# Kernel optimization log

Measured on AMD Instinct MI355X. Metric: run time of the kernel, lower is better.

Reference implementation:

```python
import jax, jax.numpy as jnp
import numpy as np

N = 100000      # nodes
E = 800000      # edges (before self-loops)
G = 128         # graphs
IN = 64         # per-table embedding dim (6 tables -> 384 input features)
L = 128         # layer_embd
OUT = 128       # out_embd
H = 2           # attention heads (concat=False -> mean over heads)
VOCABS = [33, 5, 3, 4, 2, 3]
NEG_SLOPE = 0.2
BN_EPS = 1e-5


def _seg_softmax(logits, seg, n):
    # softmax of per-edge/per-node logits grouped by segment id
    m = jax.ops.segment_max(logits, seg, num_segments=n)
    e = jnp.exp(logits - m[seg])
    s = jax.ops.segment_sum(e, seg, num_segments=n)
    return e / (s[seg] + 1e-16)


def _gat_conv(x, W, a_src, a_dst, b, src, dst, n):
    # PyG GATConv, add_self_loops already applied to (src,dst), concat=False
    h = (x @ W).reshape(n, H, -1)                 # [N,H,C]
    al_s = jnp.sum(h * a_src, axis=-1)            # [N,H]
    al_d = jnp.sum(h * a_dst, axis=-1)            # [N,H]
    e = jax.nn.leaky_relu(al_s[src] + al_d[dst], NEG_SLOPE)   # [E,H]
    alpha = _seg_softmax(e, dst, n)               # softmax over each dst's in-edges
    msg = h[src] * alpha[:, :, None]              # [E,H,C]
    out = jax.ops.segment_sum(msg, dst, num_segments=n)       # [N,H,C]
    return out.mean(axis=1) + b                   # head-mean + bias


def setup_inputs() -> dict:
    key = jax.random.key(0)
    ks = jax.random.split(key, 40)
    cols = [jax.random.randint(ks[i], (N, 1), 0, VOCABS[i]) for i in range(6)]
    x = jnp.concatenate(cols, axis=1).astype(jnp.int64)
    edge_index = jax.random.randint(ks[6], (2, E), 0, N).astype(jnp.int64)
    edge_type = jax.random.randint(ks[7], (E,), 0, 4).astype(jnp.int64)
    batch = jnp.sort(jax.random.randint(ks[8], (N,), 0, G)).astype(jnp.int64)
    s = 0.05
    p = {}
    for i in range(6):
        p[f"emb{i}"] = jax.random.normal(ks[10 + i], (VOCABS[i], IN)) * s
    p["W1"] = jax.random.normal(ks[16], (6 * IN, H * L)) * s
    p["as1"] = jax.random.normal(ks[17], (H, L)) * s
    p["ad1"] = jax.random.normal(ks[18], (H, L)) * s
    p["b1"] = jnp.zeros((L,))
    p["W2"] = jax.random.normal(ks[19], (L, H * OUT)) * s
    p["as2"] = jax.random.normal(ks[20], (H, OUT)) * s
    p["ad2"] = jax.random.normal(ks[21], (H, OUT)) * s
    p["b2"] = jnp.zeros((OUT,))
    p["gw1"] = jax.random.normal(ks[22], (OUT, OUT)) * s
    p["gb1"] = jnp.zeros((OUT,))
    p["bn_g"] = jnp.ones((OUT,))
    p["bn_b"] = jnp.zeros((OUT,))
    p["bn_m"] = jnp.zeros((OUT,))
    p["bn_v"] = jnp.ones((OUT,))
    p["gw2"] = jax.random.normal(ks[23], (OUT, 1)) * s
    p["gb2"] = jnp.zeros((1,))
    p["glw"] = jax.random.normal(ks[24], (OUT, 1)) * s
    p["glb"] = jnp.zeros((1,))
    return dict(x=x, edge_index=edge_index, edge_type=edge_type, batch=batch, **p)


def reference(x, edge_index, edge_type, batch,
              emb0, emb1, emb2, emb3, emb4, emb5,
              W1, as1, ad1, b1, W2, as2, ad2, b2,
              gw1, gb1, bn_g, bn_b, bn_m, bn_v, gw2, gb2, glw, glb):
    n = x.shape[0]
    embs = [emb0, emb1, emb2, emb3, emb4, emb5]
    x_ = jnp.concatenate([embs[i][x[:, i]] for i in range(6)], axis=1)  # [N, 6*IN]
    loops = jnp.arange(n)
    src = jnp.concatenate([edge_index[0], loops])
    dst = jnp.concatenate([edge_index[1], loops])
    out = jax.nn.sigmoid(_gat_conv(x_, W1, as1, ad1, b1, src, dst, n))
    out = jax.nn.sigmoid(_gat_conv(out, W2, as2, ad2, b2, src, dst, n))
    # GlobalAttention pooling (eval-mode BatchNorm in gate_nn)
    gh = out @ gw1 + gb1
    gh = (gh - bn_m) / jnp.sqrt(bn_v + BN_EPS) * bn_g + bn_b
    gh = jax.nn.relu(gh)
    logits = gh @ gw2 + gb2                       # [N,1]
    gate = _seg_softmax(logits, batch, G)         # softmax over nodes per graph
    pooled = jax.ops.segment_sum(gate * out, batch, num_segments=G)  # [G,OUT]
    return jax.nn.sigmoid(pooled @ glw + glb)     # [G,1]
```

## Files before the change

### kernel.cpp

```cpp
#include <hip/hip_runtime.h>
#include <hip/hip_bf16.h>
#include <hip/hip_fp16.h>

#define NN 100000
#define EE 800000
#define GG 128

typedef short bf16x8 __attribute__((ext_vector_type(8)));
typedef float f32x4 __attribute__((ext_vector_type(4)));
typedef float f32x2 __attribute__((ext_vector_type(2)));

__device__ __forceinline__ float bf2f(unsigned short v) {
    union { unsigned int u; float f; } x; x.u = ((unsigned int)v) << 16; return x.f;
}
__device__ __forceinline__ unsigned short f2bf(float f) {
    union { float f; unsigned int u; } x; x.f = f;
    unsigned int r = x.u + 0x7fffu + ((x.u >> 16) & 1u);
    return (unsigned short)(r >> 16);
}
__device__ __forceinline__ float sigmoidf_(float x) { return 1.f / (1.f + __expf(-x)); }
__device__ __forceinline__ float ldp(const void* p, int i, int f) {
    return f ? ((const float*)p)[i] : bf2f(((const unsigned short*)p)[i]);
}

#if defined(__has_builtin)
#if __has_builtin(__builtin_amdgcn_cvt_pk_f32_fp8) && __has_builtin(__builtin_amdgcn_cvt_pk_fp8_f32)
#define USE_HW_FP8 1
#endif
#endif
#ifndef USE_HW_FP8
#define USE_HW_FP8 0
#endif

#if USE_HW_FP8
__device__ __forceinline__ int fp8_pack2(float a, float b) {
    return __builtin_amdgcn_cvt_pk_fp8_f32(a, b, 0, false);
}
__device__ __forceinline__ void fp8_dec4v(unsigned int q, f32x2& lo, f32x2& hi) {
    lo = __builtin_amdgcn_cvt_pk_f32_fp8((int)q, false);
    hi = __builtin_amdgcn_cvt_pk_f32_fp8((int)q, true);
}
#else
__device__ __forceinline__ unsigned char f2bf8(float f) {
    unsigned short u = __half_as_ushort(__float2half(f));
    unsigned short r = u + 0x7f + ((u >> 8) & 1);
    return (unsigned char)(r >> 8);
}
__device__ __forceinline__ int fp8_pack2(float a, float b) {
    return (int)f2bf8(a) | ((int)f2bf8(b) << 8);
}
__device__ __forceinline__ float bf8_dec(unsigned int b) {
    return __half2float(__ushort_as_half((unsigned short)(b << 8)));
}
__device__ __forceinline__ void fp8_dec4v(unsigned int q, f32x2& lo, f32x2& hi) {
    lo[0] = bf8_dec(q & 0xff); lo[1] = bf8_dec((q >> 8) & 0xff);
    hi[0] = bf8_dec((q >> 16) & 0xff); hi[1] = bf8_dec(q >> 24);
}
#endif

__global__ void k_probe2(const unsigned int* __restrict__ w, const int* __restrict__ ei,
                         int* __restrict__ fflag, int* __restrict__ iflag) {
    __shared__ int s[256];
    int t = threadIdx.x;
    if (blockIdx.x == 0) {
        int cnt = 0;
        for (int i = t; i < 1024; i += 256) {
            unsigned int v = w[i];
            int e = (v >> 7) & 0xff;
            cnt += (e >= 100 && e <= 127) ? 1 : 0;
        }
        s[t] = cnt; __syncthreads();
        for (int d = 128; d > 0; d >>= 1) { if (t < d) s[t] += s[t + d]; __syncthreads(); }
        if (t == 0) fflag[0] = (s[0] >= 512) ? 0 : 1;
    } else {
        int nz = 0;
        for (int i = t; i < 1024; i += 256) nz |= ei[2 * i + 1];
        s[t] = nz; __syncthreads();
        for (int d = 128; d > 0; d >>= 1) { if (t < d) s[t] |= s[t + d]; __syncthreads(); }
        if (t == 0) iflag[0] = (s[0] == 0) ? 1 : 0;
    }
}

__global__ void k_cvt(const int* __restrict__ xi, const int* __restrict__ ei,
                      const int* __restrict__ bi, const int* __restrict__ flag,
                      int* __restrict__ xn, int* __restrict__ srcn,
                      int* __restrict__ dstn, int* __restrict__ batchn,
                      int* __restrict__ count) {
    int j = blockIdx.x * 256 + threadIdx.x;
    int f = flag[0];
    const int XT = NN * 6, ET = 2 * EE;
    if (j < XT) xn[j] = f ? xi[2 * j] : xi[j];
    int je = j - XT;
    if (je >= 0 && je < ET) {
        int v = f ? ei[2 * je] : ei[je];
        if (je < EE) srcn[je] = v;
        else { dstn[je - EE] = v; atomicAdd(&count[v], 1); }
    }
    int jb = j - XT - ET;
    if (jb >= 0 && jb < NN) batchn[jb] = f ? bi[2 * jb] : bi[jb];
}

__global__ void k_chunk_sum(const int* __restrict__ count, int* __restrict__ csum) {
    __shared__ int s[256];
    int t = threadIdx.x;
    int base = blockIdx.x * 1024 + t * 4;
    int acc = 0;
    #pragma unroll
    for (int j = 0; j < 4; j++) { int n = base + j; if (n < NN) acc += count[n]; }
    s[t] = acc; __syncthreads();
    for (int d = 128; d > 0; d >>= 1) { if (t < d) s[t] += s[t + d]; __syncthreads(); }
    if (t == 0) csum[blockIdx.x] = s[0];
}

__global__ void k_chunk_scan(const int* __restrict__ csum, int* __restrict__ coff, int nchunk) {
    __shared__ int s[256];
    int t = threadIdx.x;
    int v = (t < nchunk) ? csum[t] : 0;
    s[t] = v; __syncthreads();
    for (int d = 1; d < 256; d <<= 1) {
        int x = (t >= d) ? s[t - d] : 0;
        __syncthreads(); s[t] += x; __syncthreads();
    }
    if (t < nchunk) coff[t] = s[t] - v;
}

__global__ void k_scan_write(const int* __restrict__ count, const int* __restrict__ coff,
                             int* __restrict__ offset, int* __restrict__ cursor) {
    __shared__ int s[256];
    int t = threadIdx.x;
    int base = blockIdx.x * 1024 + t * 4;
    int v[4]; int acc = 0;
    #pragma unroll
    for (int j = 0; j < 4; j++) { v[j] = (base + j < NN) ? count[base + j] : 0; acc += v[j]; }
    s[t] = acc; __syncthreads();
    for (int d = 1; d < 256; d <<= 1) {
        int x = (t >= d) ? s[t - d] : 0;
        __syncthreads(); s[t] += x; __syncthreads();
    }
    int pre = s[t] - acc + coff[blockIdx.x];
    #pragma unroll
    for (int j = 0; j < 4; j++) {
        if (base + j < NN) { offset[base + j] = pre; cursor[base + j] = pre; pre += v[j]; }
    }
}

__global__ void k_scatter(const int* __restrict__ src, const int* __restrict__ dst,
                          int* __restrict__ cursor, int* __restrict__ sorted) {
    int e = blockIdx.x * 256 + threadIdx.x;
    if (e < EE) {
        int d = dst[e];
        int p = atomicAdd(&cursor[d], 1);
        sorted[p] = src[e];
    }
}

__global__ void k_cvtp(const void* W2,
                       const void* as1, const void* ad1, const void* b1,
                       const void* as2, const void* ad2, const void* b2,
                       const void* gw1, const void* gb1,
                       const void* bng, const void* bnb, const void* bnm, const void* bnv,
                       const void* gw2, const void* gb2, const void* glw, const void* glb,
                       const int* __restrict__ fflag,
                       unsigned short* __restrict__ W2T,
                       unsigned short* __restrict__ GWT, float* __restrict__ gb1p,
                       float* __restrict__ vs1, float* __restrict__ vd1,
                       float* __restrict__ vs2, float* __restrict__ vd2,
                       float* __restrict__ vb1, float* __restrict__ vb2,
                       float* __restrict__ gw2f, float* __restrict__ glwf,
                       float* __restrict__ gb2f, float* __restrict__ glbf) {
    int i = blockIdx.x * 256 + threadIdx.x;
    int f = fflag[0];
    if (i < 32768) { int k = i / 256, n = i % 256; W2T[n * 128 + k] = f2bf(ldp(W2, i, f)); }
    if (i < 16384) {
        int n = i >> 7, k = i & 127;
        float sc = ldp(bng, n, f) * rsqrtf(ldp(bnv, n, f) + 1e-5f);
        GWT[i] = f2bf(ldp(gw1, k * 128 + n, f) * sc);
    }
    if (i < 256) {
        vs1[i] = ldp(as1, i, f); vd1[i] = ldp(ad1, i, f);
        vs2[i] = ldp(as2, i, f); vd2[i] = ldp(ad2, i, f);
    }
    if (i < 128) {
        vb1[i] = ldp(b1, i, f); vb2[i] = ldp(b2, i, f);
        gw2f[i] = ldp(gw2, i, f); glwf[i] = ldp(glw, i, f);
        float sc = ldp(bng, i, f) * rsqrtf(ldp(bnv, i, f) + 1e-5f);
        gb1p[i] = (ldp(gb1, i, f) - ldp(bnm, i, f)) * sc + ldp(bnb, i, f);
    }
    if (i == 0) { gb2f[0] = ldp(gb2, 0, f); glbf[0] = ldp(glb, 0, f); }
}

__constant__ int c_vbase[7] = {0, 33, 38, 41, 45, 47, 50};
__global__ __launch_bounds__(256) void k_prep_p(
    const void* e0, const void* e1, const void* e2,
    const void* e3, const void* e4, const void* e5,
    const void* W1, const int* __restrict__ fflag,
    float* __restrict__ P) {
    int r = blockIdx.x;
    int c = threadIdx.x;
    int f = fflag[0];
    int t = 0;
    while (r >= c_vbase[t + 1]) t++;
    int v = r - c_vbase[t];
    const void* emb = (t == 0) ? e0 : (t == 1) ? e1 : (t == 2) ? e2 :
                      (t == 3) ? e3 : (t == 4) ? e4 : e5;
    float acc = 0.f;
    #pragma unroll 8
    for (int k = 0; k < 64; k++) {
        acc += ldp(emb, v * 64 + k, f) * ldp(W1, (t * 64 + k) * 256 + c, f);
    }
    P[r * 256 + c] = acc;
}

__global__ __launch_bounds__(256) void k_embsum(
    const int* __restrict__ xn, const float* __restrict__ P,
    const float* __restrict__ avs, const float* __restrict__ avd,
    unsigned char* __restrict__ H8,
    float* __restrict__ alS, float* __restrict__ alD) {
    int node = blockIdx.x * 4 + (threadIdx.x >> 6);
    if (node >= NN) return;
    int lane = threadIdx.x & 63;
    int c0 = lane * 4;
    int ix[6];
    #pragma unroll
    for (int t = 0; t < 6; t++) ix[t] = (c_vbase[t] + xn[node * 6 + t]) * 256 + c0;
    float4 a = *(const float4*)(P + ix[0]);
    #pragma unroll
    for (int t = 1; t < 6; t++) {
        float4 b = *(const float4*)(P + ix[t]);
        a.x += b.x; a.y += b.y; a.z += b.z; a.w += b.w;
    }
    float4 sv = *(const float4*)(avs + c0);
    float4 dv = *(const float4*)(avd + c0);
    float ps = a.x * sv.x + a.y * sv.y + a.z * sv.z + a.w * sv.w;
    float pd = a.x * dv.x + a.y * dv.y + a.z * dv.z + a.w * dv.w;
    #pragma unroll
    for (int m = 1; m < 32; m <<= 1) {
        ps += __shfl_xor(ps, m);
        pd += __shfl_xor(pd, m);
    }
    if ((lane & 31) == 0) {
        int head = lane >> 5;
        alS[node * 2 + head] = ps;
        alD[node * 2 + head] = pd;
    }
    unsigned int u = ((unsigned)fp8_pack2(a.x, a.y) & 0xffffu) |
                     ((unsigned)fp8_pack2(a.z, a.w) << 16);
    *(unsigned int*)(H8 + (size_t)node * 256 + c0) = u;
}

__global__ __launch_bounds__(256, 2) void k_gemm(
    const unsigned short* __restrict__ Ain,
    const unsigned short* __restrict__ WT, unsigned char* __restrict__ H8,
    const float* __restrict__ avs, const float* __restrict__ avd,
    float* __restrict__ alS, float* __restrict__ alD,
    int K)
{
    __shared__ __align__(16) unsigned short As[64 * 32];
    __shared__ __align__(16) unsigned short Bs[256 * 32];
    int tid = threadIdx.x;
    int wave = tid >> 6, lane = tid & 63;
    int quad = lane >> 4, lr = lane & 15;
    int m0 = blockIdx.x * 64;

    f32x4 zero4 = {0.f, 0.f, 0.f, 0.f};
    f32x4 acc[16];
    #pragma unroll
    for (int j = 0; j < 16; j++) acc[j] = zero4;

    for (int k0 = 0; k0 < K; k0 += 32) {
        {
            int row = tid >> 2, part = tid & 3;
            int gr = m0 + row; if (gr >= NN) gr = NN - 1;
            int g = ((row >> 4) << 6) + (part << 4) + (row & 15);
            g ^= (part << 1);
            *(uint4*)(&As[g * 8]) = *(const uint4*)(Ain + (size_t)gr * K + k0 + part * 8);
        }
        #pragma unroll
        for (int i = 0; i < 4; i++) {
            int idx = tid + i * 256;
            int row = idx >> 2, part = idx & 3;
            int g = ((row >> 4) << 6) + (part << 4) + (row & 15);
            g ^= (part << 1);
            *(uint4*)(&Bs[g * 8]) =
                *(const uint4*)(WT + (size_t)row * K + k0 + part * 8);
        }
        __syncthreads();

        int sw = (quad << 1);
        bf16x8 af0 = *(const bf16x8*)(&As[((wave * 64 + lane) ^ sw) * 8]);
        #pragma unroll
        for (int ni = 0; ni < 16; ni++) {
            bf16x8 bfv = *(const bf16x8*)(&Bs[((ni * 64 + lane) ^ sw) * 8]);
            acc[ni] = __builtin_amdgcn_mfma_f32_16x16x32_bf16(af0, bfv, acc[ni], 0, 0, 0);
        }
        __syncthreads();
    }

    float svv[16], dvv[16];
    #pragma unroll
    for (int ni = 0; ni < 16; ni++) { svv[ni] = avs[ni * 16 + lr]; dvv[ni] = avd[ni * 16 + lr]; }
    #pragma unroll
    for (int r = 0; r < 4; r++) {
        int grow = m0 + wave * 16 + quad * 4 + r;
        float ps0 = 0.f, ps1 = 0.f, pd0 = 0.f, pd1 = 0.f;
        if (grow < NN) {
            #pragma unroll
            for (int ni = 0; ni < 16; ni += 2) {
                float v0 = acc[ni][r], v1 = acc[ni + 1][r];
                int pk = fp8_pack2(v0, v1);
                H8[(size_t)grow * 256 + ni * 16 + lr] = (unsigned char)(pk & 0xff);
                H8[(size_t)grow * 256 + (ni + 1) * 16 + lr] = (unsigned char)((pk >> 8) & 0xff);
                if (ni < 8) { ps0 += v0 * svv[ni] + v1 * svv[ni + 1]; pd0 += v0 * dvv[ni] + v1 * dvv[ni + 1]; }
                else        { ps1 += v0 * svv[ni] + v1 * svv[ni + 1]; pd1 += v0 * dvv[ni] + v1 * dvv[ni + 1]; }
            }
        }
        #pragma unroll
        for (int m = 1; m < 16; m <<= 1) {
            ps0 += __shfl_xor(ps0, m); ps1 += __shfl_xor(ps1, m);
            pd0 += __shfl_xor(pd0, m); pd1 += __shfl_xor(pd1, m);
        }
        if (lr == 0 && grow < NN) {
            alS[grow * 2 + 0] = ps0; alS[grow * 2 + 1] = ps1;
            alD[grow * 2 + 0] = pd0; alD[grow * 2 + 1] = pd1;
        }
    }
}

__device__ __forceinline__ float edge_w(float e) {
    e = e > 0.f ? e : 0.2f * e;
    e = fminf(fmaxf(e, -60.f), 60.f);
    return __expf(e);
}
__global__ __launch_bounds__(256) void k_agg(const unsigned char* __restrict__ H8,
                                             const float* __restrict__ alS, const float* __restrict__ alD,
                                             const int* __restrict__ sorted, const int* __restrict__ offs,
                                             const int* __restrict__ cnts,
                                             const float* __restrict__ bias,
                                             unsigned short* __restrict__ Out) {
    __shared__ uint4 lw[4][64];
    int wid = threadIdx.x >> 6;
    int node = blockIdx.x * 4 + wid;
    if (node >= NN) return;
    int lane = threadIdx.x & 63;
    int head = lane >> 5;
    float2 adv = *(const float2*)(alD + node * 2);
    float myAd = head ? adv.y : adv.x;
    const unsigned char* Hl = H8 + lane * 4;

    float ws = edge_w(alS[node * 2 + head] + myAd);
    unsigned int qv = *(const unsigned int*)(Hl + ((unsigned)node << 8));
    f32x2 lo, hi; fp8_dec4v(qv, lo, hi);
    float den = ws;
    f32x2 wsv = {ws, ws};
    f32x2 n01 = lo * wsv, n23 = hi * wsv;

    int off = offs[node], cnt = cnts[node];
    for (int c = 0; c < cnt; c += 64) {
        int m = cnt - c; if (m > 64) m = 64;
        int j = off + c + (lane < m ? lane : 0);
        int s = sorted[j];
        float2 asv = *(const float2*)(alS + s * 2);
        float w0 = edge_w(asv.x + adv.x);
        float w1 = edge_w(asv.y + adv.y);
        lw[wid][lane] = make_uint4((unsigned)s << 8, __float_as_uint(w0), __float_as_uint(w1), 0u);
        int i = 0;
        for (; i + 8 <= m; i += 8) {
            uint4 e[8];
            #pragma unroll
            for (int u = 0; u < 8; u++) e[u] = lw[wid][i + u];
            unsigned q[8];
            #pragma unroll
            for (int u = 0; u < 8; u++) q[u] = *(const unsigned int*)(Hl + e[u].x);
            #pragma unroll
            for (int u = 0; u < 8; u++) {
                float w = __uint_as_float(head ? e[u].z : e[u].y);
                f32x2 l, h; fp8_dec4v(q[u], l, h);
                den += w;
                f32x2 wv = {w, w};
                n01 += l * wv;
                n23 += h * wv;
            }
        }
        for (; i + 4 <= m; i += 4) {
            uint4 e[4];
            #pragma unroll
            for (int u = 0; u < 4; u++) e[u] = lw[wid][i + u];
            unsigned q[4];
            #pragma unroll
            for (int u = 0; u < 4; u++) q[u] = *(const unsigned int*)(Hl + e[u].x);
            #pragma unroll
            for (int u = 0; u < 4; u++) {
                float w = __uint_as_float(head ? e[u].z : e[u].y);
                f32x2 l, h; fp8_dec4v(q[u], l, h);
                den += w;
                f32x2 wv = {w, w};
                n01 += l * wv;
                n23 += h * wv;
            }
        }
        for (; i < m; i++) {
            uint4 e0 = lw[wid][i];
            unsigned q0 = *(const unsigned int*)(Hl + e0.x);
            float w = __uint_as_float(head ? e0.z : e0.y);
            f32x2 l, h; fp8_dec4v(q0, l, h);
            den += w;
            f32x2 wv = {w, w};
            n01 += l * wv;
            n23 += h * wv;
        }
    }
    float inv = 1.f / den;
    float v0 = n01[0] * inv, v1 = n01[1] * inv, v2 = n23[0] * inv, v3 = n23[1] * inv;
    float o0 = 0.5f * (v0 + __shfl_xor(v0, 32));
    float o1 = 0.5f * (v1 + __shfl_xor(v1, 32));
    float o2 = 0.5f * (v2 + __shfl_xor(v2, 32));
    float o3 = 0.5f * (v3 + __shfl_xor(v3, 32));
    if (lane < 32) {
        int c = lane * 4;
        float4 bv = *(const float4*)(bias + c);
        o0 = sigmoidf_(o0 + bv.x);
        o1 = sigmoidf_(o1 + bv.y);
        o2 = sigmoidf_(o2 + bv.z);
        o3 = sigmoidf_(o3 + bv.w);
        uint2 pv;
        pv.x = (unsigned int)f2bf(o0) | ((unsigned int)f2bf(o1) << 16);
        pv.y = (unsigned int)f2bf(o2) | ((unsigned int)f2bf(o3) << 16);
        *(uint2*)(Out + (size_t)node * 128 + c) = pv;
    }
}

__global__ __launch_bounds__(256, 2) void k_gatemm(
    const unsigned short* __restrict__ Obuf,
    const unsigned short* __restrict__ GWT,
    const float* __restrict__ gb1p, const float* __restrict__ gw2f,
    const float* __restrict__ gb2f, float* __restrict__ logits)
{
    __shared__ __align__(16) unsigned short As[64 * 32];
    __shared__ __align__(16) unsigned short Bs[128 * 32];
    int tid = threadIdx.x;
    int wave = tid >> 6, lane = tid & 63;
    int quad = lane >> 4, lr = lane & 15;
    int m0 = blockIdx.x * 64;

    f32x4 zero4 = {0.f, 0.f, 0.f, 0.f};
    f32x4 acc[8];
    #pragma unroll
    for (int j = 0; j < 8; j++) acc[j] = zero4;

    for (int k0 = 0; k0 < 128; k0 += 32) {
        {
            int row = tid >> 2, part = tid & 3;
            int gr = m0 + row; if (gr >= NN) gr = NN - 1;
            int g = ((row >> 4) << 6) + (part << 4) + (row & 15);
            g ^= (part << 1);
            *(uint4*)(&As[g * 8]) =
                *(const uint4*)(Obuf + (size_t)gr * 128 + k0 + part * 8);
        }
        #pragma unroll
        for (int i = 0; i < 2; i++) {
            int idx = tid + i * 256;
            int row = idx >> 2, part = idx & 3;
            int g = ((row >> 4) << 6) + (part << 4) + (row & 15);
            g ^= (part << 1);
            *(uint4*)(&Bs[g * 8]) =
                *(const uint4*)(GWT + (size_t)row * 128 + k0 + part * 8);
        }
        __syncthreads();

        int sw = (quad << 1);
        bf16x8 af0 = *(const bf16x8*)(&As[((wave * 64 + lane) ^ sw) * 8]);
        #pragma unroll
        for (int ni = 0; ni < 8; ni++) {
            bf16x8 bfv = *(const bf16x8*)(&Bs[((ni * 64 + lane) ^ sw) * 8]);
            acc[ni] = __builtin_amdgcn_mfma_f32_16x16x32_bf16(af0, bfv, acc[ni], 0, 0, 0);
        }
        __syncthreads();
    }

    float gb[8], gw[8];
    #pragma unroll
    for (int ni = 0; ni < 8; ni++) { gb[ni] = gb1p[ni * 16 + lr]; gw[ni] = gw2f[ni * 16 + lr]; }
    #pragma unroll
    for (int r = 0; r < 4; r++) {
        int grow = m0 + wave * 16 + quad * 4 + r;
        float part = 0.f;
        #pragma unroll
        for (int ni = 0; ni < 8; ni++) {
            float v = acc[ni][r] + gb[ni];
            v = v > 0.f ? v : 0.f;
            part += v * gw[ni];
        }
        #pragma unroll
        for (int m = 1; m < 16; m <<= 1) part += __shfl_xor(part, m);
        if (lr == 0 && grow < NN) logits[grow] = part + gb2f[0];
    }
}

__device__ int lbound(const int* a, int n, int key) {
    int lo = 0, hi = n;
    while (lo < hi) { int mid = (lo + hi) >> 1; if (a[mid] < key) lo = mid + 1; else hi = mid; }
    return lo;
}

__global__ __launch_bounds__(256) void k_gmax(const float* __restrict__ logits,
                                              const int* __restrict__ batch,
                                              float* __restrict__ gmax) {
    __shared__ int sb[2];
    __shared__ float sm[256];
    int g = blockIdx.x, t = threadIdx.x;
    if (t < 2) sb[t] = lbound(batch, NN, g + t);
    __syncthreads();
    int lo = sb[0], hi = sb[1];
    float mx = -1e30f;
    for (int i = lo + t; i < hi; i += 256) mx = fmaxf(mx, logits[i]);
    sm[t] = mx; __syncthreads();
    for (int s = 128; s > 0; s >>= 1) { if (t < s) sm[t] = fmaxf(sm[t], sm[t + s]); __syncthreads(); }
    if (t == 0) gmax[g] = sm[0];
}

#define NPB 256
__global__ __launch_bounds__(256) void k_ppart(const unsigned short* __restrict__ Out2,
                                               const float* __restrict__ logits,
                                               const int* __restrict__ batch,
                                               const float* __restrict__ gmax,
                                               float* __restrict__ accv,
                                               float* __restrict__ accw) {
    int t = threadIdx.x;
    int c = t & 127, half = t >> 7;
    int b0 = blockIdx.x * NPB;
    int b1 = b0 + NPB; if (b1 > NN) b1 = NN;
    float acc = 0.f, aw = 0.f;
    int g = -1;
    for (int i = b0 + half; i < b1; i += 2) {
        int gi = batch[i];
        if (gi != g) {
            if (g >= 0) {
                atomicAdd(&accv[g * 128 + c], acc);
                if (c == 0) atomicAdd(&accw[g], aw);
            }
            g = gi; acc = 0.f; aw = 0.f;
        }
        float w = __expf(logits[i] - gmax[gi]);
        acc += w * bf2f(Out2[(size_t)i * 128 + c]);
        if (c == 0) aw += w;
    }
    if (g >= 0) {
        atomicAdd(&accv[g * 128 + c], acc);
        if (c == 0) atomicAdd(&accw[g], aw);
    }
}

__global__ __launch_bounds__(128) void k_pfin(const float* __restrict__ accv,
                                              const float* __restrict__ accw,
                                              const float* __restrict__ glwf,
                                              const float* __restrict__ glbf,
                                              const int* __restrict__ fflag,
                                              void* __restrict__ out) {
    __shared__ float sv[128];
    int g = blockIdx.x, t = threadIdx.x;
    float pooled = accv[g * 128 + t] / (accw[g] + 1e-16f);
    sv[t] = pooled * glwf[t];
    __syncthreads();
    for (int s = 64; s > 0; s >>= 1) { if (t < s) sv[t] += sv[t + s]; __syncthreads(); }
    if (t == 0) {
        float r = sigmoidf_(sv[0] + glbf[0]);
        if (fflag[0]) ((float*)out)[g] = r;
        else ((unsigned short*)out)[g] = f2bf(r);
    }
}

extern "C" void kernel_launch(void* const* d_in, const int* in_sizes, int n_in,
                              void* d_out, int out_size, void* d_ws, size_t ws_size,
                              hipStream_t stream) {
    const int* x_raw  = (const int*)d_in[0];
    const int* ei_raw = (const int*)d_in[1];
    const int* b_raw  = (const int*)d_in[3];

    char* p = (char*)d_ws;
    auto alloc = [&](size_t bytes) { void* r = (void*)p; p += (bytes + 255) & ~(size_t)255; return r; };
    unsigned char* H8   = (unsigned char*)alloc((size_t)NN * 256);
    unsigned short* Obuf = (unsigned short*)alloc((size_t)NN * 128 * 2);
    float* alS   = (float*)alloc((size_t)NN * 2 * 4);
    float* alD   = (float*)alloc((size_t)NN * 2 * 4);
    float* logit = (float*)alloc((size_t)NN * 4);
    char* z0 = p;
    int* count   = (int*)alloc((size_t)NN * 4);
    float* accv  = (float*)alloc(GG * 128 * 4);
    float* accw  = (float*)alloc(GG * 4);
    size_t zlen = (size_t)(p - z0);
    int* offs    = (int*)alloc((size_t)NN * 4);
    int* cursor  = (int*)alloc((size_t)NN * 4);
    int* sorted  = (int*)alloc((size_t)EE * 4);
    int* csum    = (int*)alloc(256 * 4);
    int* coff    = (int*)alloc(256 * 4);
    unsigned short* W2T  = (unsigned short*)alloc(256 * 128 * 2);
    unsigned short* GWT  = (unsigned short*)alloc(128 * 128 * 2);
    float* gb1p = (float*)alloc(128 * 4);
    float* Ptab = (float*)alloc(50 * 256 * 4);
    int* xn     = (int*)alloc((size_t)NN * 6 * 4);
    int* srcn   = (int*)alloc((size_t)EE * 4);
    int* dstn   = (int*)alloc((size_t)EE * 4);
    int* batchn = (int*)alloc((size_t)NN * 4);
    int* iflag  = (int*)alloc(256);
    int* fflag  = (int*)alloc(256);
    float* vs1  = (float*)alloc(256 * 4);
    float* vd1  = (float*)alloc(256 * 4);
    float* vs2  = (float*)alloc(256 * 4);
    float* vd2  = (float*)alloc(256 * 4);
    float* vb1  = (float*)alloc(128 * 4);
    float* vb2  = (float*)alloc(128 * 4);
    float* gw2f = (float*)alloc(128 * 4);
    float* glwf = (float*)alloc(128 * 4);
    float* gb2f = (float*)alloc(4);
    float* glbf = (float*)alloc(4);
    float* gmax = (float*)alloc(GG * 4);

    const int NCHUNK = (NN + 1023) / 1024;
    const int NBM = (NN + 63) / 64;
    const int NBE = (EE + 255) / 256;
    const int NB4 = (NN + 3) / 4;
    const int CVT_TOT = NN * 6 + 2 * EE + NN;

    hipMemsetAsync(z0, 0, zlen, stream);

    k_probe2<<<2, 256, 0, stream>>>((const unsigned int*)d_in[10], ei_raw, fflag, iflag);
    k_cvt<<<(CVT_TOT + 255) / 256, 256, 0, stream>>>(x_raw, ei_raw, b_raw, iflag,
                                                     xn, srcn, dstn, batchn, count);
    k_cvtp<<<(32768 + 255) / 256, 256, 0, stream>>>(
        d_in[14],
        d_in[11], d_in[12], d_in[13], d_in[15], d_in[16], d_in[17],
        d_in[18], d_in[19], d_in[20], d_in[21], d_in[22], d_in[23],
        d_in[24], d_in[25], d_in[26], d_in[27],
        fflag, W2T, GWT, gb1p,
        vs1, vd1, vs2, vd2, vb1, vb2, gw2f, glwf, gb2f, glbf);
    k_prep_p<<<50, 256, 0, stream>>>(d_in[4], d_in[5], d_in[6], d_in[7], d_in[8], d_in[9],
                                     d_in[10], fflag, Ptab);

    k_chunk_sum<<<NCHUNK, 256, 0, stream>>>(count, csum);
    k_chunk_scan<<<1, 256, 0, stream>>>(csum, coff, NCHUNK);
    k_scan_write<<<NCHUNK, 256, 0, stream>>>(count, coff, offs, cursor);
    k_scatter<<<NBE, 256, 0, stream>>>(srcn, dstn, cursor, sorted);

    k_embsum<<<NB4, 256, 0, stream>>>(xn, Ptab, vs1, vd1, H8, alS, alD);
    k_agg<<<NB4, 256, 0, stream>>>(H8, alS, alD, sorted, offs, count, vb1, Obuf);

    k_gemm<<<NBM, 256, 0, stream>>>(Obuf, W2T, H8, vs2, vd2, alS, alD, 128);
    k_agg<<<NB4, 256, 0, stream>>>(H8, alS, alD, sorted, offs, count, vb2, Obuf);

    k_gatemm<<<NBM, 256, 0, stream>>>(Obuf, GWT, gb1p, gw2f, gb2f, logit);
    k_gmax<<<GG, 256, 0, stream>>>(logit, batchn, gmax);
    k_ppart<<<(NN + NPB - 1) / NPB, 256, 0, stream>>>(Obuf, logit, batchn, gmax, accv, accw);
    k_pfin<<<GG, 128, 0, stream>>>(accv, accw, glwf, glbf, fflag, d_out);
}
```

Baseline: 458.1 us.

## Fuse gate GEMM with attention pooling and drop index conversion pass

Removes the separate int64-to-int32 conversion kernel: the histogram, scatter, embedding and gate kernels now read the raw index arrays directly with a stride shift. The two parameter-prep kernels are merged into one launch. The gate GEMM now loads the full 64x128 tile once into LDS and reuses it for the weighted pooling sum. This removes the logits buffer, the per-graph max kernel and the separate pooling pass. Dropping the max subtraction before exp relies on the gate logits staying small and could overflow for large values.

Result: faster. 413.3 us (-9.8%).

```diff
diff --git a/kernel.cpp b/kernel.cpp
--- a/kernel.cpp
+++ b/kernel.cpp
@@ -81,23 +81,14 @@
     }
 }
 
-__global__ void k_cvt(const int* __restrict__ xi, const int* __restrict__ ei,
-                      const int* __restrict__ bi, const int* __restrict__ flag,
-                      int* __restrict__ xn, int* __restrict__ srcn,
-                      int* __restrict__ dstn, int* __restrict__ batchn,
-                      int* __restrict__ count) {
-    int j = blockIdx.x * 256 + threadIdx.x;
-    int f = flag[0];
-    const int XT = NN * 6, ET = 2 * EE;
-    if (j < XT) xn[j] = f ? xi[2 * j] : xi[j];
-    int je = j - XT;
-    if (je >= 0 && je < ET) {
-        int v = f ? ei[2 * je] : ei[je];
-        if (je < EE) srcn[je] = v;
-        else { dstn[je - EE] = v; atomicAdd(&count[v], 1); }
-    }
-    int jb = j - XT - ET;
-    if (jb >= 0 && jb < NN) batchn[jb] = f ? bi[2 * jb] : bi[jb];
+__global__ void k_hist(const int* __restrict__ ei, const int* __restrict__ iflag,
+                       int* __restrict__ count) {
+    int e = blockIdx.x * 256 + threadIdx.x;
+    if (e < EE) {
+        int f = iflag[0];
+        int d = ei[(EE + e) << f];
+        atomicAdd(&count[d], 1);
+    }
 }
 
 __global__ void k_chunk_sum(const int* __restrict__ count, int* __restrict__ csum) {
@@ -144,32 +135,55 @@
     }
 }
 
-__global__ void k_scatter(const int* __restrict__ src, const int* __restrict__ dst,
+__global__ void k_scatter(const int* __restrict__ ei, const int* __restrict__ iflag,
                           int* __restrict__ cursor, int* __restrict__ sorted) {
     int e = blockIdx.x * 256 + threadIdx.x;
     if (e < EE) {
-        int d = dst[e];
+        int f = iflag[0];
+        int s = ei[e << f];
+        int d = ei[(EE + e) << f];
         int p = atomicAdd(&cursor[d], 1);
-        sorted[p] = src[e];
-    }
-}
-
-__global__ void k_cvtp(const void* W2,
-                       const void* as1, const void* ad1, const void* b1,
-                       const void* as2, const void* ad2, const void* b2,
-                       const void* gw1, const void* gb1,
-                       const void* bng, const void* bnb, const void* bnm, const void* bnv,
-                       const void* gw2, const void* gb2, const void* glw, const void* glb,
-                       const int* __restrict__ fflag,
-                       unsigned short* __restrict__ W2T,
-                       unsigned short* __restrict__ GWT, float* __restrict__ gb1p,
-                       float* __restrict__ vs1, float* __restrict__ vd1,
-                       float* __restrict__ vs2, float* __restrict__ vd2,
-                       float* __restrict__ vb1, float* __restrict__ vb2,
-                       float* __restrict__ gw2f, float* __restrict__ glwf,
-                       float* __restrict__ gb2f, float* __restrict__ glbf) {
+        sorted[p] = s;
+    }
+}
+
+__constant__ int c_vbase[7] = {0, 33, 38, 41, 45, 47, 50};
+__global__ __launch_bounds__(256) void k_prep(
+    const void* e0, const void* e1, const void* e2,
+    const void* e3, const void* e4, const void* e5,
+    const void* W1, const void* W2,
+    const void* as1, const void* ad1, const void* b1,
+    const void* as2, const void* ad2, const void* b2,
+    const void* gw1, const void* gb1,
+    const void* bng, const void* bnb, const void* bnm, const void* bnv,
+    const void* gw2, const void* gb2, const void* glw, const void* glb,
+    const int* __restrict__ fflag,
+    unsigned short* __restrict__ W2T,
+    unsigned short* __restrict__ GWT, float* __restrict__ gb1p,
+    float* __restrict__ vs1, float* __restrict__ vd1,
+    float* __restrict__ vs2, float* __restrict__ vd2,
+    float* __restrict__ vb1, float* __restrict__ vb2,
+    float* __restrict__ gw2f, float* __restrict__ glwf,
+    float* __restrict__ gb2f, float* __restrict__ glbf,
+    float* __restrict__ P) {
+    int f = fflag[0];
+    if (blockIdx.x >= 128) {
+        int r = blockIdx.x - 128;
+        int c = threadIdx.x;
+        int t = 0;
+        while (r >= c_vbase[t + 1]) t++;
+        int v = r - c_vbase[t];
+        const void* emb = (t == 0) ? e0 : (t == 1) ? e1 : (t == 2) ? e2 :
+                          (t == 3) ? e3 : (t == 4) ? e4 : e5;
+        float acc = 0.f;
+        #pragma unroll 8
+        for (int k = 0; k < 64; k++) {
+            acc += ldp(emb, v * 64 + k, f) * ldp(W1, (t * 64 + k) * 256 + c, f);
+        }
+        P[r * 256 + c] = acc;
+        return;
+    }
     int i = blockIdx.x * 256 + threadIdx.x;
-    int f = fflag[0];
     if (i < 32768) { int k = i / 256, n = i % 256; W2T[n * 128 + k] = f2bf(ldp(W2, i, f)); }
     if (i < 16384) {
         int n = i >> 7, k = i & 127;
@@ -189,40 +203,20 @@
     if (i == 0) { gb2f[0] = ldp(gb2, 0, f); glbf[0] = ldp(glb, 0, f); }
 }
 
-__constant__ int c_vbase[7] = {0, 33, 38, 41, 45, 47, 50};
-__global__ __launch_bounds__(256) void k_prep_p(
-    const void* e0, const void* e1, const void* e2,
-    const void* e3, const void* e4, const void* e5,
-    const void* W1, const int* __restrict__ fflag,
-    float* __restrict__ P) {
-    int r = blockIdx.x;
-    int c = threadIdx.x;
-    int f = fflag[0];
-    int t = 0;
-    while (r >= c_vbase[t + 1]) t++;
-    int v = r - c_vbase[t];
-    const void* emb = (t == 0) ? e0 : (t == 1) ? e1 : (t == 2) ? e2 :
-                      (t == 3) ? e3 : (t == 4) ? e4 : e5;
-    float acc = 0.f;
-    #pragma unroll 8
-    for (int k = 0; k < 64; k++) {
-        acc += ldp(emb, v * 64 + k, f) * ldp(W1, (t * 64 + k) * 256 + c, f);
-    }
-    P[r * 256 + c] = acc;
-}
-
 __global__ __launch_bounds__(256) void k_embsum(
-    const int* __restrict__ xn, const float* __restrict__ P,
+    const int* __restrict__ x_raw, const int* __restrict__ iflag,
+    const float* __restrict__ P,
     const float* __restrict__ avs, const float* __restrict__ avd,
     unsigned char* __restrict__ H8,
     float* __restrict__ alS, float* __restrict__ alD) {
     int node = blockIdx.x * 4 + (threadIdx.x >> 6);
     if (node >= NN) return;
+    int f = iflag[0];
     int lane = threadIdx.x & 63;
     int c0 = lane * 4;
     int ix[6];
     #pragma unroll
-    for (int t = 0; t < 6; t++) ix[t] = (c_vbase[t] + xn[node * 6 + t]) * 256 + c0;
+    for (int t = 0; t < 6; t++) ix[t] = (c_vbase[t] + x_raw[(node * 6 + t) << f]) * 256 + c0;
     float4 a = *(const float4*)(P + ix[0]);
     #pragma unroll
     for (int t = 1; t < 6; t++) {
@@ -429,52 +423,61 @@
     }
 }
 
-__global__ __launch_bounds__(256, 2) void k_gatemm(
+__global__ __launch_bounds__(256, 2) void k_gate(
     const unsigned short* __restrict__ Obuf,
     const unsigned short* __restrict__ GWT,
     const float* __restrict__ gb1p, const float* __restrict__ gw2f,
-    const float* __restrict__ gb2f, float* __restrict__ logits)
+    const float* __restrict__ gb2f,
+    const int* __restrict__ batch_raw, const int* __restrict__ iflag,
+    float* __restrict__ accv, float* __restrict__ accw)
 {
-    __shared__ __align__(16) unsigned short As[64 * 32];
-    __shared__ __align__(16) unsigned short Bs[128 * 32];
+    __shared__ __align__(16) unsigned short As[64 * 128];
+    __shared__ __align__(16) unsigned short Bs[128 * 128];
+    __shared__ float wlds[64];
+    __shared__ int gid[64];
     int tid = threadIdx.x;
     int wave = tid >> 6, lane = tid & 63;
     int quad = lane >> 4, lr = lane & 15;
     int m0 = blockIdx.x * 64;
 
+    #pragma unroll
+    for (int i = 0; i < 4; i++) {
+        int idx = tid + i * 256;
+        int row = idx >> 4, p = idx & 15;
+        int gr = m0 + row; if (gr >= NN) gr = NN - 1;
+        int slot = row * 16 + (p & 8) + ((p & 7) ^ (row & 7));
+        *(uint4*)(&As[slot * 8]) = *(const uint4*)(Obuf + (size_t)gr * 128 + p * 8);
+    }
+    #pragma unroll
+    for (int i = 0; i < 8; i++) {
+        int idx = tid + i * 256;
+        int row = idx >> 4, p = idx & 15;
+        int slot = row * 16 + (p & 8) + ((p & 7) ^ (row & 7));
+        *(uint4*)(&Bs[slot * 8]) = *(const uint4*)(GWT + (size_t)row * 128 + p * 8);
+    }
+    if (tid < 64) {
+        int nd = m0 + tid; if (nd >= NN) nd = NN - 1;
+        gid[tid] = batch_raw[nd << iflag[0]];
+    }
+    __syncthreads();
+
     f32x4 zero4 = {0.f, 0.f, 0.f, 0.f};
     f32x4 acc[8];
     #pragma unroll
     for (int j = 0; j < 8; j++) acc[j] = zero4;
 
+    int rowa = wave * 16 + lr;
+    #pragma unroll
     for (int k0 = 0; k0 < 128; k0 += 32) {
-        {
-            int row = tid >> 2, part = tid & 3;
-            int gr = m0 + row; if (gr >= NN) gr = NN - 1;
-            int g = ((row >> 4) << 6) + (part << 4) + (row & 15);
-            g ^= (part << 1);
-            *(uint4*)(&As[g * 8]) =
-                *(const uint4*)(Obuf + (size_t)gr * 128 + k0 + part * 8);
-        }
-        #pragma unroll
-        for (int i = 0; i < 2; i++) {
-            int idx = tid + i * 256;
-            int row = idx >> 2, part = idx & 3;
-            int g = ((row >> 4) << 6) + (part << 4) + (row & 15);
-            g ^= (part << 1);
-            *(uint4*)(&Bs[g * 8]) =
-                *(const uint4*)(GWT + (size_t)row * 128 + k0 + part * 8);
-        }
-        __syncthreads();
-
-        int sw = (quad << 1);
-        bf16x8 af0 = *(const bf16x8*)(&As[((wave * 64 + lane) ^ sw) * 8]);
+        int kb = k0 >> 3;
+        int pa = (kb & 8) + (((kb & 7) + quad) ^ (lr & 7));
+        bf16x8 af0 = *(const bf16x8*)(&As[(rowa * 16 + pa) * 8]);
         #pragma unroll
         for (int ni = 0; ni < 8; ni++) {
-            bf16x8 bfv = *(const bf16x8*)(&Bs[((ni * 64 + lane) ^ sw) * 8]);
+            int rowb = ni * 16 + lr;
+            bf16x8 bfv = *(const bf16x8*)(&Bs[(rowb * 16 + pa) * 8]);
             acc[ni] = __builtin_amdgcn_mfma_f32_16x16x32_bf16(af0, bfv, acc[ni], 0, 0, 0);
         }
-        __syncthreads();
     }
 
     float gb[8], gw[8];
@@ -482,7 +485,7 @@
     for (int ni = 0; ni < 8; ni++) { gb[ni] = gb1p[ni * 16 + lr]; gw[ni] = gw2f[ni * 16 + lr]; }
     #pragma unroll
     for (int r = 0; r < 4; r++) {
-        int grow = m0 + wave * 16 + quad * 4 + r;
+        int row = wave * 16 + quad * 4 + r;
         float part = 0.f;
         #pragma unroll
         for (int ni = 0; ni < 8; ni++) {
@@ -492,61 +495,37 @@
         }
         #pragma unroll
         for (int m = 1; m < 16; m <<= 1) part += __shfl_xor(part, m);
-        if (lr == 0 && grow < NN) logits[grow] = part + gb2f[0];
-    }
-}
-
-__device__ int lbound(const int* a, int n, int key) {
-    int lo = 0, hi = n;
-    while (lo < hi) { int mid = (lo + hi) >> 1; if (a[mid] < key) lo = mid + 1; else hi = mid; }
-    return lo;
-}
-
-__global__ __launch_bounds__(256) void k_gmax(const float* __restrict__ logits,
-                                              const int* __restrict__ batch,
-                                              float* __restrict__ gmax) {
-    __shared__ int sb[2];
-    __shared__ float sm[256];
-    int g = blockIdx.x, t = threadIdx.x;
-    if (t < 2) sb[t] = lbound(batch, NN, g + t);
+        if (lr == 0) {
+            float w = (m0 + row < NN) ? __expf(part + gb2f[0]) : 0.f;
+            wlds[row] = w;
+        }
+    }
     __syncthreads();
-    int lo = sb[0], hi = sb[1];
-    float mx = -1e30f;
-    for (int i = lo + t; i < hi; i += 256) mx = fmaxf(mx, logits[i]);
-    sm[t] = mx; __syncthreads();
-    for (int s = 128; s > 0; s >>= 1) { if (t < s) sm[t] = fmaxf(sm[t], sm[t + s]); __syncthreads(); }
-    if (t == 0) gmax[g] = sm[0];
-}
-
-#define NPB 256
-__global__ __launch_bounds__(256) void k_ppart(const unsigned short* __restrict__ Out2,
-                                               const float* __restrict__ logits,
-                                               const int* __restrict__ batch,
-                                               const float* __restrict__ gmax,
-                                               float* __restrict__ accv,
-                                               float* __restrict__ accw) {
-    int t = threadIdx.x;
-    int c = t & 127, half = t >> 7;
-    int b0 = blockIdx.x * NPB;
-    int b1 = b0 + NPB; if (b1 > NN) b1 = NN;
-    float acc = 0.f, aw = 0.f;
+
+    int ch = tid & 127;
+    int r0 = (tid >> 7) * 32;
+    int p = ch >> 3, ip = ch & 7;
+    float accum = 0.f, aw = 0.f;
     int g = -1;
-    for (int i = b0 + half; i < b1; i += 2) {
-        int gi = batch[i];
+    for (int rr = 0; rr < 32; rr++) {
+        int row = r0 + rr;
+        int gi = gid[row];
+        float w = wlds[row];
         if (gi != g) {
             if (g >= 0) {
-                atomicAdd(&accv[g * 128 + c], acc);
-                if (c == 0) atomicAdd(&accw[g], aw);
+                atomicAdd(&accv[g * 128 + ch], accum);
+                if (ch == 0) atomicAdd(&accw[g], aw);
             }
-            g = gi; acc = 0.f; aw = 0.f;
-        }
-        float w = __expf(logits[i] - gmax[gi]);
-        acc += w * bf2f(Out2[(size_t)i * 128 + c]);
-        if (c == 0) aw += w;
+            g = gi; accum = 0.f; aw = 0.f;
+        }
+        int slot = row * 16 + (p & 8) + ((p & 7) ^ (row & 7));
+        float val = bf2f(As[slot * 8 + ip]);
+        accum += w * val;
+        if (ch == 0) aw += w;
     }
     if (g >= 0) {
-        atomicAdd(&accv[g * 128 + c], acc);
-        if (c == 0) atomicAdd(&accw[g], aw);
+        atomicAdd(&accv[g * 128 + ch], accum);
+        if (ch == 0) atomicAdd(&accw[g], aw);
     }
 }
 
@@ -582,7 +561,6 @@
     unsigned short* Obuf = (unsigned short*)alloc((size_t)NN * 128 * 2);
     float* alS   = (float*)alloc((size_t)NN * 2 * 4);
     float* alD   = (float*)alloc((size_t)NN * 2 * 4);
-    float* logit = (float*)alloc((size_t)NN * 4);
     char* z0 = p;
     int* count   = (int*)alloc((size_t)NN * 4);
     float* accv  = (float*)alloc(GG * 128 * 4);
@@ -597,10 +575,6 @@
     unsigned short* GWT  = (unsigned short*)alloc(128 * 128 * 2);
     float* gb1p = (float*)alloc(128 * 4);
     float* Ptab = (float*)alloc(50 * 256 * 4);
-    int* xn     = (int*)alloc((size_t)NN * 6 * 4);
-    int* srcn   = (int*)alloc((size_t)EE * 4);
-    int* dstn   = (int*)alloc((size_t)EE * 4);
-    int* batchn = (int*)alloc((size_t)NN * 4);
     int* iflag  = (int*)alloc(256);
     int* fflag  = (int*)alloc(256);
     float* vs1  = (float*)alloc(256 * 4);
@@ -613,42 +587,36 @@
     float* glwf = (float*)alloc(128 * 4);
     float* gb2f = (float*)alloc(4);
     float* glbf = (float*)alloc(4);
-    float* gmax = (float*)alloc(GG * 4);
 
     const int NCHUNK = (NN + 1023) / 1024;
     const int NBM = (NN + 63) / 64;
     const int NBE = (EE + 255) / 256;
     const int NB4 = (NN + 3) / 4;
-    const int CVT_TOT = NN * 6 + 2 * EE + NN;
 
     hipMemsetAsync(z0, 0, zlen, stream);
 
     k_probe2<<<2, 256, 0, stream>>>((const unsigned int*)d_in[10], ei_raw, fflag, iflag);
-    k_cvt<<<(CVT_TOT + 255) / 256, 256, 0, stream>>>(x_raw, ei_raw, b_raw, iflag,
-                                                     xn, srcn, dstn, batchn, count);
-    k_cvtp<<<(32768 + 255) / 256, 256, 0, stream>>>(
-        d_in[14],
+    k_hist<<<NBE, 256, 0, stream>>>(ei_raw, iflag, count);
+    k_prep<<<178, 256, 0, stream>>>(
+        d_in[4], d_in[5], d_in[6], d_in[7], d_in[8], d_in[9],
+        d_in[10], d_in[14],
         d_in[11], d_in[12], d_in[13], d_in[15], d_in[16], d_in[17],
         d_in[18], d_in[19], d_in[20], d_in[21], d_in[22], d_in[23],
         d_in[24], d_in[25], d_in[26], d_in[27],
         fflag, W2T, GWT, gb1p,
-        vs1, vd1, vs2, vd2, vb1, vb2, gw2f, glwf, gb2f, glbf);
-    k_prep_p<<<50, 256, 0, stream>>>(d_in[4], d_in[5], d_in[6], d_in[7], d_in[8], d_in[9],
-                                     d_in[10], fflag, Ptab);
+        vs1, vd1, vs2, vd2, vb1, vb2, gw2f, glwf, gb2f, glbf, Ptab);
 
     k_chunk_sum<<<NCHUNK, 256, 0, stream>>>(count, csum);
     k_chunk_scan<<<1, 256, 0, stream>>>(csum, coff, NCHUNK);
     k_scan_write<<<NCHUNK, 256, 0, stream>>>(count, coff, offs, cursor);
-    k_scatter<<<NBE, 256, 0, stream>>>(srcn, dstn, cursor, sorted);
-
-    k_embsum<<<NB4, 256, 0, stream>>>(xn, Ptab, vs1, vd1, H8, alS, alD);
+    k_scatter<<<NBE, 256, 0, stream>>>(ei_raw, iflag, cursor, sorted);
+
+    k_embsum<<<NB4, 256, 0, stream>>>(x_raw, iflag, Ptab, vs1, vd1, H8, alS, alD);
     k_agg<<<NB4, 256, 0, stream>>>(H8, alS, alD, sorted, offs, count, vb1, Obuf);
 
     k_gemm<<<NBM, 256, 0, stream>>>(Obuf, W2T, H8, vs2, vd2, alS, alD, 128);
     k_agg<<<NB4, 256, 0, stream>>>(H8, alS, alD, sorted, offs, count, vb2, Obuf);
 
-    k_gatemm<<<NBM, 256, 0, stream>>>(Obuf, GWT, gb1p, gw2f, gb2f, logit);
-    k_gmax<<<GG, 256, 0, stream>>>(logit, batchn, gmax);
-    k_ppart<<<(NN + NPB - 1) / NPB, 256, 0, stream>>>(Obuf, logit, batchn, gmax, accv, accw);
+    k_gate<<<NBM, 256, 0, stream>>>(Obuf, GWT, gb1p, gw2f, gb2f, b_raw, iflag, accv, accw);
     k_pfin<<<GG, 128, 0, stream>>>(accv, accw, glwf, glbf, fflag, d_out);
 }
```
